# Kernel optimization log

Hardware: AMD Instinct MI355X
Metric: run time of the kernel (lower is better)

Reference implementation:

```python
import jax, jax.numpy as jnp
import numpy as np

N_NODES = 2048
N_PAIRS = 65536
D = 512
P = 16


def setup_inputs() -> dict:
    key = jax.random.key(0)
    ks = jax.random.split(key, 9)
    scale = 1.0 / np.sqrt(D)
    obj_feats = jax.random.normal(ks[0], (N_NODES, D), dtype=jnp.float32)
    union_feats = jax.random.normal(ks[1], (N_PAIRS, D), dtype=jnp.float32)
    pair_idxs = jax.random.randint(ks[2], (N_PAIRS, 2), 0, N_NODES, dtype=jnp.int64)
    ws_w = jax.random.uniform(ks[3], (D, D), jnp.float32, -scale, scale)
    ws_b = jax.random.uniform(ks[4], (D,), jnp.float32, -scale, scale)
    wo_w = jax.random.uniform(ks[5], (D, D), jnp.float32, -scale, scale)
    wo_b = jax.random.uniform(ks[6], (D,), jnp.float32, -scale, scale)
    w_w = jax.random.uniform(ks[7], (P, D), jnp.float32, -scale, scale)
    w_b = jax.random.uniform(ks[8], (P,), jnp.float32, -scale, scale)
    return {
        'obj_feats': obj_feats, 'union_feats': union_feats, 'pair_idxs': pair_idxs,
        'ws_w': ws_w, 'ws_b': ws_b, 'wo_w': wo_w, 'wo_b': wo_b, 'w_w': w_w, 'w_b': w_b,
    }


def reference(obj_feats, union_feats, pair_idxs, ws_w, ws_b, wo_w, wo_b, w_w, w_b):
    n = obj_feats.shape[0]
    p = w_w.shape[0]
    # node projections: [N, D]
    s = obj_feats @ ws_w.T + ws_b
    o = obj_feats @ wo_w.T + wo_b
    # gather pair features and fuse elementwise product: [E, D]
    prod = s[pair_idxs[:, 0]] * o[pair_idxs[:, 1]] * union_feats
    # project to p attention logits per pair: [E, p]
    atten_f = prod @ w_w.T + w_b
    # scatter into dense [N, N, p]
    atten = jnp.zeros((n, n, p), dtype=obj_feats.dtype)
    atten = atten.at[pair_idxs[:, 0], pair_idxs[:, 1]].add(atten_f)
    # mask diagonal with -1e4 and softmax over axis=1 (incoming nodes)
    atten = atten - jnp.eye(n, dtype=obj_feats.dtype)[:, :, None] * 10000.0
    return jax.nn.softmax(atten, axis=1)
```

## Files before the change

### kernel.cpp

```cpp
#include <hip/hip_runtime.h>
#include <hip/hip_bf16.h>

#define N_NODES 2048
#define N_PAIRS 65536
#define DIM 512
#define NP 16
#define SLOTS 96

typedef __attribute__((ext_vector_type(8))) short s16x8;
typedef __attribute__((ext_vector_type(8))) unsigned short u16x8;
typedef __attribute__((ext_vector_type(4))) float f32x4;

static __device__ __forceinline__ unsigned short f2bf(float x) {
    union { float f; unsigned int u; } v; v.f = x;
    unsigned int r = v.u + 0x7FFFu + ((v.u >> 16) & 1u);
    return (unsigned short)(r >> 16);
}
static __device__ __forceinline__ float bf2f(unsigned short u) {
    union { unsigned int u; float f; } v; v.u = ((unsigned int)u) << 16;
    return v.f;
}
static __device__ __forceinline__ u16x8 pack8(float4 a, float4 b) {
    u16x8 r;
    r[0]=f2bf(a.x); r[1]=f2bf(a.y); r[2]=f2bf(a.z); r[3]=f2bf(a.w);
    r[4]=f2bf(b.x); r[5]=f2bf(b.y); r[6]=f2bf(b.z); r[7]=f2bf(b.w);
    return r;
}

#define GBM 64
#define GBN 64
#define GBK 32
#define GSA 40

__global__ __launch_bounds__(256) void gemm_so(
    const float* __restrict__ A, const float* __restrict__ Ws, const float* __restrict__ bsv,
    const float* __restrict__ Wo, const float* __restrict__ bov,
    unsigned short* __restrict__ Sb, unsigned short* __restrict__ Ob)
{
    __shared__ unsigned short As[GBM*GSA];
    __shared__ unsigned short Bs[GBN*GSA];
    const int tid = threadIdx.x;
    const int m0 = blockIdx.y*GBM, n0 = blockIdx.x*GBN;
    const int ar = tid>>2, ac = (tid&3)*8;
    const float* Arow = A + (size_t)(m0+ar)*DIM + ac;
    const int nrow = n0 + ar;
    const float* Wrow = (nrow < DIM ? Ws + (size_t)nrow*DIM : Wo + (size_t)(nrow-DIM)*DIM) + ac;
    float4 a_r[2], b_r[2];
    a_r[0] = *(const float4*)(Arow);   a_r[1] = *(const float4*)(Arow+4);
    b_r[0] = *(const float4*)(Wrow);   b_r[1] = *(const float4*)(Wrow+4);

    const int lane = tid&63, wid = tid>>6;
    const int wm = (wid>>1)*32, wn = (wid&1)*32;
    const int fr = lane&15, ks8 = (lane>>4)*8;
    f32x4 acc[2][2] = {};
    for (int k0=0; k0<DIM; k0+=GBK) {
        *(u16x8*)&As[ar*GSA+ac] = pack8(a_r[0],a_r[1]);
        *(u16x8*)&Bs[ar*GSA+ac] = pack8(b_r[0],b_r[1]);
        __syncthreads();
        if (k0+GBK < DIM) {
            a_r[0] = *(const float4*)(Arow + k0+GBK);   a_r[1] = *(const float4*)(Arow + k0+GBK + 4);
            b_r[0] = *(const float4*)(Wrow + k0+GBK);   b_r[1] = *(const float4*)(Wrow + k0+GBK + 4);
        }
        s16x8 af[2], bfr[2];
        #pragma unroll
        for (int mi=0;mi<2;++mi) af[mi]  = *(const s16x8*)&As[(wm+mi*16+fr)*GSA + ks8];
        #pragma unroll
        for (int ni=0;ni<2;++ni) bfr[ni] = *(const s16x8*)&Bs[(wn+ni*16+fr)*GSA + ks8];
        #pragma unroll
        for (int mi=0;mi<2;++mi)
            #pragma unroll
            for (int ni=0;ni<2;++ni)
                acc[mi][ni] = __builtin_amdgcn_mfma_f32_16x16x32_bf16(af[mi], bfr[ni], acc[mi][ni], 0,0,0);
        __syncthreads();
    }
    const int rg = lane>>4;
    #pragma unroll
    for (int ni=0;ni<2;++ni) {
        const int n = n0 + wn + ni*16 + fr;
        const float bias = (n < DIM) ? bsv[n] : bov[n-DIM];
        unsigned short* dst = (n < DIM) ? (Sb + n) : (Ob + (n - DIM));
        #pragma unroll
        for (int mi=0;mi<2;++mi) {
            #pragma unroll
            for (int q=0;q<4;++q) {
                const int m = m0 + wm + mi*16 + rg*4 + q;
                dst[(size_t)m*DIM] = f2bf(acc[mi][ni][q] + bias);
            }
        }
    }
}

#define SP 520

__global__ __launch_bounds__(256) void pairproj_k(
    const unsigned short* __restrict__ Sb, const unsigned short* __restrict__ Ob,
    const float* __restrict__ U, const int* __restrict__ idx,
    const float* __restrict__ w_w, const float* __restrict__ w_b,
    int* __restrict__ rowcnt, int* __restrict__ rowj, float* __restrict__ rowv)
{
    __shared__ unsigned short P[4*16*SP];
    const int tid = threadIdx.x;
    const int lane = tid&63, wid = tid>>6;
    const int fr = lane&15, ks8 = (lane>>4)*8;
    s16x8 wreg[16];
    #pragma unroll
    for (int st=0;st<16;++st) {
        const float4* wp = (const float4*)(w_w + (size_t)fr*DIM + st*32 + ks8);
        u16x8 t = pack8(wp[0], wp[1]);
        wreg[st] = *(s16x8*)&t;
    }
    const float wbv = w_b[fr];
    unsigned short* Pw = &P[wid*16*SP];
    const int eb = blockIdx.x*128 + wid*32;
    for (int it=0; it<2; ++it) {
        const int e0 = eb + it*16;
        #pragma unroll 4
        for (int s8=0; s8<16; ++s8) {
            const int e = e0 + s8;
            const int i = idx[2*e], j = idx[2*e+1];
            u16x8 sv = *(const u16x8*)(Sb + (size_t)i*DIM + lane*8);
            u16x8 ov = *(const u16x8*)(Ob + (size_t)j*DIM + lane*8);
            const float4* up = (const float4*)(U + (size_t)e*DIM + lane*8);
            float4 u0 = up[0], u1 = up[1];
            float4 p0, p1;
            p0.x = bf2f(sv[0])*bf2f(ov[0])*u0.x;
            p0.y = bf2f(sv[1])*bf2f(ov[1])*u0.y;
            p0.z = bf2f(sv[2])*bf2f(ov[2])*u0.z;
            p0.w = bf2f(sv[3])*bf2f(ov[3])*u0.w;
            p1.x = bf2f(sv[4])*bf2f(ov[4])*u1.x;
            p1.y = bf2f(sv[5])*bf2f(ov[5])*u1.y;
            p1.z = bf2f(sv[6])*bf2f(ov[6])*u1.z;
            p1.w = bf2f(sv[7])*bf2f(ov[7])*u1.w;
            *(u16x8*)&Pw[s8*SP + lane*8] = pack8(p0, p1);
        }
        f32x4 acc = {0.f,0.f,0.f,0.f};
        #pragma unroll
        for (int st=0;st<16;++st) {
            s16x8 af = *(const s16x8*)&Pw[fr*SP + st*32 + ks8];
            acc = __builtin_amdgcn_mfma_f32_16x16x32_bf16(af, wreg[st], acc, 0,0,0);
        }
        int iv = 0, posv = 0;
        if (lane < 16) {
            const int e = e0 + lane;
            iv = idx[2*e];
            const int jv = idx[2*e + 1];
            posv = atomicAdd(&rowcnt[iv], 1);
            if (posv < SLOTS) rowj[iv*SLOTS + posv] = jv;
        }
        const int rg = lane>>4;
        #pragma unroll
        for (int q=0;q<4;++q) {
            const int pr = rg*4 + q;
            const int ip = __shfl(iv, pr, 64);
            const int pp = __shfl(posv, pr, 64);
            if (pp < SLOTS)
                rowv[((size_t)ip*SLOTS + pp)*NP + fr] = acc[q] + wbv;
        }
    }
}

__global__ __launch_bounds__(256) void softmax_k(
    const int* __restrict__ rowcnt, const int* __restrict__ rowj,
    const float* __restrict__ rowv, float* __restrict__ out)
{
    __shared__ __align__(16) float vals[SLOTS][NP];
    __shared__ int jcol[SLOTS];
    __shared__ unsigned char dead[SLOTS];
    __shared__ float red[16][17];
    __shared__ float mP[NP], invZ[NP], bg[NP];
    __shared__ int ndistinct;
    const int i = blockIdx.x;
    const int t = threadIdx.x;
    int c = rowcnt[i];
    if (c > SLOTS) c = SLOTS;

    if (t == 0) ndistinct = 0;
    for (int a = t; a < c; a += 256) {
        jcol[a] = rowj[i*SLOTS + a];
        dead[a] = 0;
        const float4* src = (const float4*)(rowv + ((size_t)i*SLOTS + a)*NP);
        float4* dst = (float4*)vals[a];
        dst[0] = src[0]; dst[1] = src[1]; dst[2] = src[2]; dst[3] = src[3];
    }
    __syncthreads();

    for (int a = t; a < c; a += 256) {
        int j = jcol[a];
        int first = a;
        for (int b = 0; b < a; ++b) if (jcol[b] == j) { first = b; break; }
        if (first != a) {
            dead[a] = 1;
            #pragma unroll
            for (int p = 0; p < NP; ++p) atomicAdd(&vals[first][p], vals[a][p]);
        }
    }
    __syncthreads();

    for (int a = t; a < c; a += 256)
        if (!dead[a] && jcol[a] != i) atomicAdd(&ndistinct, 1);
    __syncthreads();

    const int p = t & 15, ch = t >> 4;
    float pm = 0.f;
    for (int a = ch; a < c; a += 16)
        if (!dead[a] && jcol[a] != i) pm = fmaxf(pm, vals[a][p]);
    red[ch][p] = pm;
    __syncthreads();
    if (t < NP) {
        float m = 0.f;
        #pragma unroll
        for (int k = 0; k < 16; ++k) m = fmaxf(m, red[k][p]);
        mP[p] = m;
    }
    __syncthreads();
    {
        const float m = mP[p];
        float ps = 0.f;
        for (int a = ch; a < c; a += 16)
            if (!dead[a] && jcol[a] != i) ps += __expf(vals[a][p] - m);
        red[ch][p] = ps;
    }
    __syncthreads();
    if (t < NP) {
        float zs = 0.f;
        #pragma unroll
        for (int k = 0; k < 16; ++k) zs += red[k][p];
        const float m = mP[p];
        const float eb = __expf(-m);
        const float nbg = (float)(N_NODES - 1 - ndistinct);
        const float Z = zs + nbg * eb;
        const float iz = 1.0f / Z;
        invZ[p] = iz; bg[p] = eb * iz;
    }
    __syncthreads();

    const size_t rowbase = (size_t)i * N_NODES * NP;
    {
        const int g = t & 3;
        float4 b4 = make_float4(bg[g*4+0], bg[g*4+1], bg[g*4+2], bg[g*4+3]);
        float4* orow = (float4*)(out + rowbase);
        #pragma unroll 8
        for (int n = 0; n < 32; ++n) orow[t + 256 * n] = b4;
    }
    __syncthreads();

    for (int a = t; a < c; a += 256) {
        if (dead[a]) continue;
        const int j = jcol[a];
        float4* dst = (float4*)(out + rowbase + (size_t)j * NP);
        if (j == i) {
            float4 z = make_float4(0.f, 0.f, 0.f, 0.f);
            dst[0] = z; dst[1] = z; dst[2] = z; dst[3] = z;
        } else {
            #pragma unroll
            for (int q = 0; q < 4; ++q) {
                float4 v;
                v.x = __expf(vals[a][4*q+0] - mP[4*q+0]) * invZ[4*q+0];
                v.y = __expf(vals[a][4*q+1] - mP[4*q+1]) * invZ[4*q+1];
                v.z = __expf(vals[a][4*q+2] - mP[4*q+2]) * invZ[4*q+2];
                v.w = __expf(vals[a][4*q+3] - mP[4*q+3]) * invZ[4*q+3];
                dst[q] = v;
            }
        }
    }
    if (t == 0) {
        float4 z = make_float4(0.f, 0.f, 0.f, 0.f);
        float4* dst = (float4*)(out + rowbase + (size_t)i * NP);
        dst[0] = z; dst[1] = z; dst[2] = z; dst[3] = z;
    }
}

extern "C" void kernel_launch(void* const* d_in, const int* in_sizes, int n_in,
                              void* d_out, int out_size, void* d_ws, size_t ws_size,
                              hipStream_t stream)
{
    (void)in_sizes; (void)n_in; (void)out_size; (void)ws_size;
    const float* obj  = (const float*)d_in[0];
    const float* uni  = (const float*)d_in[1];
    const int*   idx  = (const int*)  d_in[2];
    const float* ws_w = (const float*)d_in[3];
    const float* ws_b = (const float*)d_in[4];
    const float* wo_w = (const float*)d_in[5];
    const float* wo_b = (const float*)d_in[6];
    const float* w_w  = (const float*)d_in[7];
    const float* w_b  = (const float*)d_in[8];
    float* out = (float*)d_out;

    unsigned short* Sb = (unsigned short*)d_ws;
    unsigned short* Ob = Sb + (size_t)N_NODES * DIM;
    float* rowv = (float*)(Ob + (size_t)N_NODES * DIM);
    int* rowj   = (int*)(rowv + (size_t)N_NODES * SLOTS * NP);
    int* rowcnt = rowj + (size_t)N_NODES * SLOTS;

    hipMemsetAsync(rowcnt, 0, N_NODES * sizeof(int), stream);
    gemm_so<<<dim3(1024/GBN, N_NODES/GBM), 256, 0, stream>>>(obj, ws_w, ws_b, wo_w, wo_b, Sb, Ob);
    pairproj_k<<<N_PAIRS/128, 256, 0, stream>>>(Sb, Ob, uni, idx, w_w, w_b, rowcnt, rowj, rowv);
    softmax_k<<<N_NODES, 256, 0, stream>>>(rowcnt, rowj, rowv, out);
}
```

Before: 130.9 us.

## Fuse pair projection and row softmax into persistent kernel with per-row readiness counters

```diff
diff --git a/kernel.cpp b/kernel.cpp
--- a/kernel.cpp
+++ b/kernel.cpp
@@ -6,6 +6,8 @@
 #define DIM 512
 #define NP 16
 #define SLOTS 96
+#define SP 520
+#define NCHUNKA (N_PAIRS/64)
 
 typedef __attribute__((ext_vector_type(8))) short s16x8;
 typedef __attribute__((ext_vector_type(8))) unsigned short u16x8;
@@ -90,183 +92,192 @@
     }
 }
 
-#define SP 520
-
-__global__ __launch_bounds__(256) void pairproj_k(
+__global__ __launch_bounds__(256) void hist_k(const int* __restrict__ idx, int* __restrict__ hist)
+{
+    int e = blockIdx.x * 256 + threadIdx.x;
+    atomicAdd(&hist[idx[2*e]], 1);
+}
+
+__global__ __launch_bounds__(128) void fused_k(
     const unsigned short* __restrict__ Sb, const unsigned short* __restrict__ Ob,
     const float* __restrict__ U, const int* __restrict__ idx,
     const float* __restrict__ w_w, const float* __restrict__ w_b,
-    int* __restrict__ rowcnt, int* __restrict__ rowj, float* __restrict__ rowv)
+    int* __restrict__ rowcnt, int* __restrict__ rowdone, const int* __restrict__ hist,
+    int* __restrict__ rowj, float* __restrict__ rowv,
+    int* __restrict__ tickets, float* __restrict__ out)
 {
-    __shared__ unsigned short P[4*16*SP];
+    __shared__ __align__(16) unsigned char smem[2*16*SP*2];
+    __shared__ int tkA, tkB, ndv;
+    __shared__ float mPv[NP], invZv[NP];
+
     const int tid = threadIdx.x;
-    const int lane = tid&63, wid = tid>>6;
-    const int fr = lane&15, ks8 = (lane>>4)*8;
-    s16x8 wreg[16];
-    #pragma unroll
-    for (int st=0;st<16;++st) {
-        const float4* wp = (const float4*)(w_w + (size_t)fr*DIM + st*32 + ks8);
-        u16x8 t = pack8(wp[0], wp[1]);
-        wreg[st] = *(s16x8*)&t;
+    const int lane = tid & 63, wid = tid >> 6;
+    const int fr = lane & 15, ks8 = (lane >> 4) * 8;
+
+    {
+        s16x8 wreg[16];
+        #pragma unroll
+        for (int st=0;st<16;++st) {
+            const float4* wp = (const float4*)(w_w + (size_t)fr*DIM + st*32 + ks8);
+            u16x8 t = pack8(wp[0], wp[1]);
+            wreg[st] = *(s16x8*)&t;
+        }
+        const float wbv = w_b[fr];
+        unsigned short* P = (unsigned short*)smem;
+        unsigned short* Pw = &P[wid*16*SP];
+        for (;;) {
+            __syncthreads();
+            if (tid == 0) tkA = atomicAdd(&tickets[0], 1);
+            __syncthreads();
+            const int chunk = tkA;
+            if (chunk >= NCHUNKA) break;
+            const int eb = chunk*64 + wid*32;
+            for (int it = 0; it < 2; ++it) {
+                const int e0 = eb + it*16;
+                #pragma unroll 4
+                for (int s8=0; s8<16; ++s8) {
+                    const int e = e0 + s8;
+                    const int i = idx[2*e], j = idx[2*e+1];
+                    u16x8 sv = *(const u16x8*)(Sb + (size_t)i*DIM + lane*8);
+                    u16x8 ov = *(const u16x8*)(Ob + (size_t)j*DIM + lane*8);
+                    const float4* up = (const float4*)(U + (size_t)e*DIM + lane*8);
+                    float4 u0 = up[0], u1 = up[1];
+                    float4 p0, p1;
+                    p0.x = bf2f(sv[0])*bf2f(ov[0])*u0.x;
+                    p0.y = bf2f(sv[1])*bf2f(ov[1])*u0.y;
+                    p0.z = bf2f(sv[2])*bf2f(ov[2])*u0.z;
+                    p0.w = bf2f(sv[3])*bf2f(ov[3])*u0.w;
+                    p1.x = bf2f(sv[4])*bf2f(ov[4])*u1.x;
+                    p1.y = bf2f(sv[5])*bf2f(ov[5])*u1.y;
+                    p1.z = bf2f(sv[6])*bf2f(ov[6])*u1.z;
+                    p1.w = bf2f(sv[7])*bf2f(ov[7])*u1.w;
+                    *(u16x8*)&Pw[s8*SP + lane*8] = pack8(p0, p1);
+                }
+                f32x4 acc = {0.f,0.f,0.f,0.f};
+                #pragma unroll
+                for (int st=0;st<16;++st) {
+                    s16x8 af = *(const s16x8*)&Pw[fr*SP + st*32 + ks8];
+                    acc = __builtin_amdgcn_mfma_f32_16x16x32_bf16(af, wreg[st], acc, 0,0,0);
+                }
+                int iv = 0, posv = 0;
+                if (lane < 16) {
+                    const int e = e0 + lane;
+                    iv = idx[2*e];
+                    const int jv = idx[2*e + 1];
+                    posv = atomicAdd(&rowcnt[iv], 1);
+                    if (posv < SLOTS) rowj[iv*SLOTS + posv] = jv;
+                }
+                const int rg = lane>>4;
+                #pragma unroll
+                for (int q=0;q<4;++q) {
+                    const int pr = rg*4 + q;
+                    const int ip = __shfl(iv, pr, 64);
+                    const int pp = __shfl(posv, pr, 64);
+                    if (pp < SLOTS)
+                        rowv[((size_t)ip*SLOTS + pp)*NP + fr] = acc[q] + wbv;
+                }
+                __threadfence();
+                if (lane < 16)
+                    __hip_atomic_fetch_add(&rowdone[iv], 1, __ATOMIC_RELEASE, __HIP_MEMORY_SCOPE_AGENT);
+            }
+        }
     }
-    const float wbv = w_b[fr];
-    unsigned short* Pw = &P[wid*16*SP];
-    const int eb = blockIdx.x*128 + wid*32;
-    for (int it=0; it<2; ++it) {
-        const int e0 = eb + it*16;
-        #pragma unroll 4
-        for (int s8=0; s8<16; ++s8) {
-            const int e = e0 + s8;
-            const int i = idx[2*e], j = idx[2*e+1];
-            u16x8 sv = *(const u16x8*)(Sb + (size_t)i*DIM + lane*8);
-            u16x8 ov = *(const u16x8*)(Ob + (size_t)j*DIM + lane*8);
-            const float4* up = (const float4*)(U + (size_t)e*DIM + lane*8);
-            float4 u0 = up[0], u1 = up[1];
-            float4 p0, p1;
-            p0.x = bf2f(sv[0])*bf2f(ov[0])*u0.x;
-            p0.y = bf2f(sv[1])*bf2f(ov[1])*u0.y;
-            p0.z = bf2f(sv[2])*bf2f(ov[2])*u0.z;
-            p0.w = bf2f(sv[3])*bf2f(ov[3])*u0.w;
-            p1.x = bf2f(sv[4])*bf2f(ov[4])*u1.x;
-            p1.y = bf2f(sv[5])*bf2f(ov[5])*u1.y;
-            p1.z = bf2f(sv[6])*bf2f(ov[6])*u1.z;
-            p1.w = bf2f(sv[7])*bf2f(ov[7])*u1.w;
-            *(u16x8*)&Pw[s8*SP + lane*8] = pack8(p0, p1);
-        }
-        f32x4 acc = {0.f,0.f,0.f,0.f};
-        #pragma unroll
-        for (int st=0;st<16;++st) {
-            s16x8 af = *(const s16x8*)&Pw[fr*SP + st*32 + ks8];
-            acc = __builtin_amdgcn_mfma_f32_16x16x32_bf16(af, wreg[st], acc, 0,0,0);
-        }
-        int iv = 0, posv = 0;
-        if (lane < 16) {
-            const int e = e0 + lane;
-            iv = idx[2*e];
-            const int jv = idx[2*e + 1];
-            posv = atomicAdd(&rowcnt[iv], 1);
-            if (posv < SLOTS) rowj[iv*SLOTS + posv] = jv;
-        }
-        const int rg = lane>>4;
-        #pragma unroll
-        for (int q=0;q<4;++q) {
-            const int pr = rg*4 + q;
-            const int ip = __shfl(iv, pr, 64);
-            const int pp = __shfl(posv, pr, 64);
-            if (pp < SLOTS)
-                rowv[((size_t)ip*SLOTS + pp)*NP + fr] = acc[q] + wbv;
-        }
-    }
-}
-
-__global__ __launch_bounds__(256) void softmax_k(
-    const int* __restrict__ rowcnt, const int* __restrict__ rowj,
-    const float* __restrict__ rowv, float* __restrict__ out)
-{
-    __shared__ __align__(16) float vals[SLOTS][NP];
-    __shared__ int jcol[SLOTS];
-    __shared__ unsigned char dead[SLOTS];
-    __shared__ float red[16][17];
-    __shared__ float mP[NP], invZ[NP], bg[NP];
-    __shared__ int ndistinct;
-    const int i = blockIdx.x;
-    const int t = threadIdx.x;
-    int c = rowcnt[i];
-    if (c > SLOTS) c = SLOTS;
-
-    if (t == 0) ndistinct = 0;
-    for (int a = t; a < c; a += 256) {
-        jcol[a] = rowj[i*SLOTS + a];
-        dead[a] = 0;
-        const float4* src = (const float4*)(rowv + ((size_t)i*SLOTS + a)*NP);
-        float4* dst = (float4*)vals[a];
-        dst[0] = src[0]; dst[1] = src[1]; dst[2] = src[2]; dst[3] = src[3];
-    }
-    __syncthreads();
-
-    for (int a = t; a < c; a += 256) {
-        int j = jcol[a];
-        int first = a;
-        for (int b = 0; b < a; ++b) if (jcol[b] == j) { first = b; break; }
-        if (first != a) {
-            dead[a] = 1;
+
+    float* vals = (float*)smem;
+    int*   jcol = (int*)(smem + 98*NP*4);
+    unsigned char* deadf = (unsigned char*)(smem + 98*NP*4 + SLOTS*4);
+    unsigned char* cmap  = deadf + SLOTS;
+    float* red = (float*)(smem + 8800);
+
+    for (;;) {
+        __syncthreads();
+        if (tid == 0) tkB = atomicAdd(&tickets[1], 1);
+        __syncthreads();
+        const int r = tkB;
+        if (r >= N_NODES) break;
+        const int expect = hist[r];
+        {
+            int g = 0;
+            while (__hip_atomic_load(&rowdone[r], __ATOMIC_ACQUIRE, __HIP_MEMORY_SCOPE_AGENT) < expect
+                   && g < (1<<25)) { ++g; __builtin_amdgcn_s_sleep(2); }
+        }
+        int c = expect; if (c > SLOTS) c = SLOTS;
+        if (tid == 0) ndv = 0;
+        for (int n = tid; n < N_NODES; n += 128) cmap[n] = (unsigned char)SLOTS;
+        for (int a = tid; a < c; a += 128) {
+            jcol[a] = rowj[r*SLOTS + a];
+            deadf[a] = 0;
+            const float4* src = (const float4*)(rowv + ((size_t)r*SLOTS + a)*NP);
+            float4* dst = (float4*)&vals[a*NP];
+            dst[0]=src[0]; dst[1]=src[1]; dst[2]=src[2]; dst[3]=src[3];
+        }
+        __syncthreads();
+        for (int a = tid; a < c; a += 128) {
+            int j = jcol[a]; int first = a;
+            for (int b = 0; b < a; ++b) if (jcol[b] == j) { first = b; break; }
+            if (first != a) {
+                deadf[a] = 1;
+                #pragma unroll
+                for (int p = 0; p < NP; ++p) atomicAdd(&vals[first*NP+p], vals[a*NP+p]);
+            }
+        }
+        __syncthreads();
+        for (int a = tid; a < c; a += 128)
+            if (!deadf[a] && jcol[a] != r) atomicAdd(&ndv, 1);
+        __syncthreads();
+        const int p = tid & 15, ch = tid >> 4;
+        float pm = 0.f;
+        for (int a = ch; a < c; a += 8)
+            if (!deadf[a] && jcol[a] != r) pm = fmaxf(pm, vals[a*NP+p]);
+        red[ch*17+p] = pm;
+        __syncthreads();
+        if (tid < NP) {
+            float m = 0.f;
             #pragma unroll
-            for (int p = 0; p < NP; ++p) atomicAdd(&vals[first][p], vals[a][p]);
-        }
-    }
-    __syncthreads();
-
-    for (int a = t; a < c; a += 256)
-        if (!dead[a] && jcol[a] != i) atomicAdd(&ndistinct, 1);
-    __syncthreads();
-
-    const int p = t & 15, ch = t >> 4;
-    float pm = 0.f;
-    for (int a = ch; a < c; a += 16)
-        if (!dead[a] && jcol[a] != i) pm = fmaxf(pm, vals[a][p]);
-    red[ch][p] = pm;
-    __syncthreads();
-    if (t < NP) {
-        float m = 0.f;
-        #pragma unroll
-        for (int k = 0; k < 16; ++k) m = fmaxf(m, red[k][p]);
-        mP[p] = m;
-    }
-    __syncthreads();
-    {
-        const float m = mP[p];
-        float ps = 0.f;
-        for (int a = ch; a < c; a += 16)
-            if (!dead[a] && jcol[a] != i) ps += __expf(vals[a][p] - m);
-        red[ch][p] = ps;
-    }
-    __syncthreads();
-    if (t < NP) {
-        float zs = 0.f;
-        #pragma unroll
-        for (int k = 0; k < 16; ++k) zs += red[k][p];
-        const float m = mP[p];
-        const float eb = __expf(-m);
-        const float nbg = (float)(N_NODES - 1 - ndistinct);
-        const float Z = zs + nbg * eb;
-        const float iz = 1.0f / Z;
-        invZ[p] = iz; bg[p] = eb * iz;
-    }
-    __syncthreads();
-
-    const size_t rowbase = (size_t)i * N_NODES * NP;
-    {
-        const int g = t & 3;
-        float4 b4 = make_float4(bg[g*4+0], bg[g*4+1], bg[g*4+2], bg[g*4+3]);
-        float4* orow = (float4*)(out + rowbase);
+            for (int k = 0; k < 8; ++k) m = fmaxf(m, red[k*17+tid]);
+            mPv[tid] = m;
+        }
+        __syncthreads();
+        {
+            const float m = mPv[p];
+            float ps = 0.f;
+            for (int a = ch; a < c; a += 8)
+                if (!deadf[a] && jcol[a] != r) ps += __expf(vals[a*NP+p] - m);
+            red[ch*17+p] = ps;
+        }
+        __syncthreads();
+        if (tid < NP) {
+            float zs = 0.f;
+            #pragma unroll
+            for (int k = 0; k < 8; ++k) zs += red[k*17+tid];
+            const float m = mPv[tid];
+            const float eb2 = __expf(-m);
+            const float Z = zs + (float)(N_NODES - 1 - ndv) * eb2;
+            const float iz = 1.0f / Z;
+            invZv[tid] = iz;
+            vals[SLOTS*NP + tid] = eb2 * iz;
+            vals[(SLOTS+1)*NP + tid] = 0.f;
+        }
+        __syncthreads();
+        for (int a = tid; a < c; a += 128) {
+            if (!deadf[a] && jcol[a] != r) {
+                #pragma unroll
+                for (int p2 = 0; p2 < NP; ++p2)
+                    vals[a*NP+p2] = __expf(vals[a*NP+p2] - mPv[p2]) * invZv[p2];
+                cmap[jcol[a]] = (unsigned char)a;
+            }
+        }
+        __syncthreads();
+        if (tid == 0) cmap[r] = (unsigned char)(SLOTS+1);
+        __syncthreads();
+        float4* orow = (float4*)(out + (size_t)r * N_NODES * NP);
+        const float4* v4 = (const float4*)vals;
         #pragma unroll 8
-        for (int n = 0; n < 32; ++n) orow[t + 256 * n] = b4;
-    }
-    __syncthreads();
-
-    for (int a = t; a < c; a += 256) {
-        if (dead[a]) continue;
-        const int j = jcol[a];
-        float4* dst = (float4*)(out + rowbase + (size_t)j * NP);
-        if (j == i) {
-            float4 z = make_float4(0.f, 0.f, 0.f, 0.f);
-            dst[0] = z; dst[1] = z; dst[2] = z; dst[3] = z;
-        } else {
-            #pragma unroll
-            for (int q = 0; q < 4; ++q) {
-                float4 v;
-                v.x = __expf(vals[a][4*q+0] - mP[4*q+0]) * invZ[4*q+0];
-                v.y = __expf(vals[a][4*q+1] - mP[4*q+1]) * invZ[4*q+1];
-                v.z = __expf(vals[a][4*q+2] - mP[4*q+2]) * invZ[4*q+2];
-                v.w = __expf(vals[a][4*q+3] - mP[4*q+3]) * invZ[4*q+3];
-                dst[q] = v;
-            }
-        }
-    }
-    if (t == 0) {
-        float4 z = make_float4(0.f, 0.f, 0.f, 0.f);
-        float4* dst = (float4*)(out + rowbase + (size_t)i * NP);
-        dst[0] = z; dst[1] = z; dst[2] = z; dst[3] = z;
+        for (int n = 0; n < 64; ++n) {
+            const int i4 = tid + 128*n;
+            const int col = i4 >> 2, q = i4 & 3;
+            orow[i4] = v4[(int)cmap[col]*4 + q];
+        }
     }
 }
 
@@ -288,12 +299,16 @@
 
     unsigned short* Sb = (unsigned short*)d_ws;
     unsigned short* Ob = Sb + (size_t)N_NODES * DIM;
-    float* rowv = (float*)(Ob + (size_t)N_NODES * DIM);
-    int* rowj   = (int*)(rowv + (size_t)N_NODES * SLOTS * NP);
-    int* rowcnt = rowj + (size_t)N_NODES * SLOTS;
-
-    hipMemsetAsync(rowcnt, 0, N_NODES * sizeof(int), stream);
+    float* rowv  = (float*)(Ob + (size_t)N_NODES * DIM);
+    int* rowj    = (int*)(rowv + (size_t)N_NODES * SLOTS * NP);
+    int* rowcnt  = rowj + (size_t)N_NODES * SLOTS;
+    int* rowdone = rowcnt + N_NODES;
+    int* hist    = rowdone + N_NODES;
+    int* tickets = hist + N_NODES;
+
+    hipMemsetAsync(rowcnt, 0, (3 * N_NODES + 8) * sizeof(int), stream);
+    hist_k<<<N_PAIRS/256, 256, 0, stream>>>(idx, hist);
     gemm_so<<<dim3(1024/GBN, N_NODES/GBM), 256, 0, stream>>>(obj, ws_w, ws_b, wo_w, wo_b, Sb, Ob);
-    pairproj_k<<<N_PAIRS/128, 256, 0, stream>>>(Sb, Ob, uni, idx, w_w, w_b, rowcnt, rowj, rowv);
-    softmax_k<<<N_NODES, 256, 0, stream>>>(rowcnt, rowj, rowv, out);
-}
+    fused_k<<<1024, 128, 0, stream>>>(Sb, Ob, uni, idx, w_w, w_b,
+                                      rowcnt, rowdone, hist, rowj, rowv, tickets, out);
+}
```

Result: slower. 432.9 us (+230.7%).

## Feed MFMA directly from gathered pair rows and write softmax rows via column map

Applied to the files above, without the earlier changes.

```diff
diff --git a/kernel.cpp b/kernel.cpp
--- a/kernel.cpp
+++ b/kernel.cpp
@@ -90,72 +90,63 @@
     }
 }
 
-#define SP 520
-
 __global__ __launch_bounds__(256) void pairproj_k(
     const unsigned short* __restrict__ Sb, const unsigned short* __restrict__ Ob,
     const float* __restrict__ U, const int* __restrict__ idx,
     const float* __restrict__ w_w, const float* __restrict__ w_b,
     int* __restrict__ rowcnt, int* __restrict__ rowj, float* __restrict__ rowv)
 {
-    __shared__ unsigned short P[4*16*SP];
     const int tid = threadIdx.x;
-    const int lane = tid&63, wid = tid>>6;
-    const int fr = lane&15, ks8 = (lane>>4)*8;
+    const int lane = tid & 63, wid = tid >> 6;
+    const int fr = lane & 15, ks8 = (lane >> 4) * 8;
     s16x8 wreg[16];
     #pragma unroll
-    for (int st=0;st<16;++st) {
+    for (int st = 0; st < 16; ++st) {
         const float4* wp = (const float4*)(w_w + (size_t)fr*DIM + st*32 + ks8);
         u16x8 t = pack8(wp[0], wp[1]);
         wreg[st] = *(s16x8*)&t;
     }
     const float wbv = w_b[fr];
-    unsigned short* Pw = &P[wid*16*SP];
-    const int eb = blockIdx.x*128 + wid*32;
-    for (int it=0; it<2; ++it) {
-        const int e0 = eb + it*16;
-        #pragma unroll 4
-        for (int s8=0; s8<16; ++s8) {
-            const int e = e0 + s8;
-            const int i = idx[2*e], j = idx[2*e+1];
-            u16x8 sv = *(const u16x8*)(Sb + (size_t)i*DIM + lane*8);
-            u16x8 ov = *(const u16x8*)(Ob + (size_t)j*DIM + lane*8);
-            const float4* up = (const float4*)(U + (size_t)e*DIM + lane*8);
-            float4 u0 = up[0], u1 = up[1];
-            float4 p0, p1;
-            p0.x = bf2f(sv[0])*bf2f(ov[0])*u0.x;
-            p0.y = bf2f(sv[1])*bf2f(ov[1])*u0.y;
-            p0.z = bf2f(sv[2])*bf2f(ov[2])*u0.z;
-            p0.w = bf2f(sv[3])*bf2f(ov[3])*u0.w;
-            p1.x = bf2f(sv[4])*bf2f(ov[4])*u1.x;
-            p1.y = bf2f(sv[5])*bf2f(ov[5])*u1.y;
-            p1.z = bf2f(sv[6])*bf2f(ov[6])*u1.z;
-            p1.w = bf2f(sv[7])*bf2f(ov[7])*u1.w;
-            *(u16x8*)&Pw[s8*SP + lane*8] = pack8(p0, p1);
-        }
-        f32x4 acc = {0.f,0.f,0.f,0.f};
-        #pragma unroll
-        for (int st=0;st<16;++st) {
-            s16x8 af = *(const s16x8*)&Pw[fr*SP + st*32 + ks8];
-            acc = __builtin_amdgcn_mfma_f32_16x16x32_bf16(af, wreg[st], acc, 0,0,0);
-        }
-        int iv = 0, posv = 0;
-        if (lane < 16) {
-            const int e = e0 + lane;
-            iv = idx[2*e];
-            const int jv = idx[2*e + 1];
-            posv = atomicAdd(&rowcnt[iv], 1);
-            if (posv < SLOTS) rowj[iv*SLOTS + posv] = jv;
-        }
-        const int rg = lane>>4;
-        #pragma unroll
-        for (int q=0;q<4;++q) {
-            const int pr = rg*4 + q;
-            const int ip = __shfl(iv, pr, 64);
-            const int pp = __shfl(posv, pr, 64);
-            if (pp < SLOTS)
-                rowv[((size_t)ip*SLOTS + pp)*NP + fr] = acc[q] + wbv;
-        }
+
+    const int e = blockIdx.x * 64 + wid * 16 + fr;
+    const int i = idx[2*e], j = idx[2*e + 1];
+    const unsigned short* sp = Sb + (size_t)i * DIM;
+    const unsigned short* op = Ob + (size_t)j * DIM;
+    const float*          up = U  + (size_t)e * DIM;
+
+    f32x4 acc = {0.f, 0.f, 0.f, 0.f};
+    #pragma unroll 4
+    for (int st = 0; st < 16; ++st) {
+        const int k = st*32 + ks8;
+        u16x8 sv = *(const u16x8*)(sp + k);
+        u16x8 ov = *(const u16x8*)(op + k);
+        float4 u0 = *(const float4*)(up + k);
+        float4 u1 = *(const float4*)(up + k + 4);
+        float4 p0, p1;
+        p0.x = bf2f(sv[0])*bf2f(ov[0])*u0.x;
+        p0.y = bf2f(sv[1])*bf2f(ov[1])*u0.y;
+        p0.z = bf2f(sv[2])*bf2f(ov[2])*u0.z;
+        p0.w = bf2f(sv[3])*bf2f(ov[3])*u0.w;
+        p1.x = bf2f(sv[4])*bf2f(ov[4])*u1.x;
+        p1.y = bf2f(sv[5])*bf2f(ov[5])*u1.y;
+        p1.z = bf2f(sv[6])*bf2f(ov[6])*u1.z;
+        p1.w = bf2f(sv[7])*bf2f(ov[7])*u1.w;
+        u16x8 pa = pack8(p0, p1);
+        acc = __builtin_amdgcn_mfma_f32_16x16x32_bf16(*(s16x8*)&pa, wreg[st], acc, 0,0,0);
+    }
+    int posv = 0;
+    if (lane < 16) {
+        posv = atomicAdd(&rowcnt[i], 1);
+        if (posv < SLOTS) rowj[i*SLOTS + posv] = j;
+    }
+    const int rg = lane >> 4;
+    #pragma unroll
+    for (int q = 0; q < 4; ++q) {
+        const int pr = rg*4 + q;
+        const int ip = __shfl(i, pr, 64);
+        const int pp = __shfl(posv, pr, 64);
+        if (pp < SLOTS)
+            rowv[((size_t)ip*SLOTS + pp)*NP + fr] = acc[q] + wbv;
     }
 }
 
@@ -163,110 +154,97 @@
     const int* __restrict__ rowcnt, const int* __restrict__ rowj,
     const float* __restrict__ rowv, float* __restrict__ out)
 {
-    __shared__ __align__(16) float vals[SLOTS][NP];
+    __shared__ __align__(16) float vals[(SLOTS+2)*NP];
     __shared__ int jcol[SLOTS];
-    __shared__ unsigned char dead[SLOTS];
+    __shared__ unsigned char deadf[SLOTS];
+    __shared__ unsigned char cmap[N_NODES];
     __shared__ float red[16][17];
-    __shared__ float mP[NP], invZ[NP], bg[NP];
-    __shared__ int ndistinct;
-    const int i = blockIdx.x;
+    __shared__ float mPv[NP], invZv[NP];
+    __shared__ int ndv;
+    const int r = blockIdx.x;
     const int t = threadIdx.x;
-    int c = rowcnt[i];
+    int c = rowcnt[r];
     if (c > SLOTS) c = SLOTS;
 
-    if (t == 0) ndistinct = 0;
+    if (t == 0) ndv = 0;
+    for (int n = t; n < N_NODES; n += 256) cmap[n] = (unsigned char)SLOTS;
     for (int a = t; a < c; a += 256) {
-        jcol[a] = rowj[i*SLOTS + a];
-        dead[a] = 0;
-        const float4* src = (const float4*)(rowv + ((size_t)i*SLOTS + a)*NP);
-        float4* dst = (float4*)vals[a];
-        dst[0] = src[0]; dst[1] = src[1]; dst[2] = src[2]; dst[3] = src[3];
+        jcol[a] = rowj[r*SLOTS + a];
+        deadf[a] = 0;
+        const float4* src = (const float4*)(rowv + ((size_t)r*SLOTS + a)*NP);
+        float4* dst = (float4*)&vals[a*NP];
+        dst[0]=src[0]; dst[1]=src[1]; dst[2]=src[2]; dst[3]=src[3];
     }
     __syncthreads();
 
     for (int a = t; a < c; a += 256) {
-        int j = jcol[a];
-        int first = a;
+        int j = jcol[a]; int first = a;
         for (int b = 0; b < a; ++b) if (jcol[b] == j) { first = b; break; }
         if (first != a) {
-            dead[a] = 1;
-            #pragma unroll
-            for (int p = 0; p < NP; ++p) atomicAdd(&vals[first][p], vals[a][p]);
-        }
-    }
-    __syncthreads();
-
+            deadf[a] = 1;
+            #pragma unroll
+            for (int p = 0; p < NP; ++p) atomicAdd(&vals[first*NP+p], vals[a*NP+p]);
+        }
+    }
+    __syncthreads();
     for (int a = t; a < c; a += 256)
-        if (!dead[a] && jcol[a] != i) atomicAdd(&ndistinct, 1);
+        if (!deadf[a] && jcol[a] != r) atomicAdd(&ndv, 1);
     __syncthreads();
 
     const int p = t & 15, ch = t >> 4;
     float pm = 0.f;
     for (int a = ch; a < c; a += 16)
-        if (!dead[a] && jcol[a] != i) pm = fmaxf(pm, vals[a][p]);
+        if (!deadf[a] && jcol[a] != r) pm = fmaxf(pm, vals[a*NP+p]);
     red[ch][p] = pm;
     __syncthreads();
     if (t < NP) {
         float m = 0.f;
         #pragma unroll
-        for (int k = 0; k < 16; ++k) m = fmaxf(m, red[k][p]);
-        mP[p] = m;
+        for (int k = 0; k < 16; ++k) m = fmaxf(m, red[k][t]);
+        mPv[t] = m;
     }
     __syncthreads();
     {
-        const float m = mP[p];
+        const float m = mPv[p];
         float ps = 0.f;
         for (int a = ch; a < c; a += 16)
-            if (!dead[a] && jcol[a] != i) ps += __expf(vals[a][p] - m);
+            if (!deadf[a] && jcol[a] != r) ps += __expf(vals[a*NP+p] - m);
         red[ch][p] = ps;
     }
     __syncthreads();
     if (t < NP) {
         float zs = 0.f;
         #pragma unroll
-        for (int k = 0; k < 16; ++k) zs += red[k][p];
-        const float m = mP[p];
+        for (int k = 0; k < 16; ++k) zs += red[k][t];
+        const float m = mPv[t];
         const float eb = __expf(-m);
-        const float nbg = (float)(N_NODES - 1 - ndistinct);
-        const float Z = zs + nbg * eb;
+        const float Z = zs + (float)(N_NODES - 1 - ndv) * eb;
         const float iz = 1.0f / Z;
-        invZ[p] = iz; bg[p] = eb * iz;
-    }
-    __syncthreads();
-
-    const size_t rowbase = (size_t)i * N_NODES * NP;
-    {
-        const int g = t & 3;
-        float4 b4 = make_float4(bg[g*4+0], bg[g*4+1], bg[g*4+2], bg[g*4+3]);
-        float4* orow = (float4*)(out + rowbase);
-        #pragma unroll 8
-        for (int n = 0; n < 32; ++n) orow[t + 256 * n] = b4;
+        invZv[t] = iz;
+        vals[SLOTS*NP + t] = eb * iz;
+        vals[(SLOTS+1)*NP + t] = 0.f;
     }
     __syncthreads();
 
     for (int a = t; a < c; a += 256) {
-        if (dead[a]) continue;
-        const int j = jcol[a];
-        float4* dst = (float4*)(out + rowbase + (size_t)j * NP);
-        if (j == i) {
-            float4 z = make_float4(0.f, 0.f, 0.f, 0.f);
-            dst[0] = z; dst[1] = z; dst[2] = z; dst[3] = z;
-        } else {
-            #pragma unroll
-            for (int q = 0; q < 4; ++q) {
-                float4 v;
-                v.x = __expf(vals[a][4*q+0] - mP[4*q+0]) * invZ[4*q+0];
-                v.y = __expf(vals[a][4*q+1] - mP[4*q+1]) * invZ[4*q+1];
-                v.z = __expf(vals[a][4*q+2] - mP[4*q+2]) * invZ[4*q+2];
-                v.w = __expf(vals[a][4*q+3] - mP[4*q+3]) * invZ[4*q+3];
-                dst[q] = v;
-            }
-        }
-    }
-    if (t == 0) {
-        float4 z = make_float4(0.f, 0.f, 0.f, 0.f);
-        float4* dst = (float4*)(out + rowbase + (size_t)i * NP);
-        dst[0] = z; dst[1] = z; dst[2] = z; dst[3] = z;
+        if (!deadf[a] && jcol[a] != r) {
+            #pragma unroll
+            for (int p2 = 0; p2 < NP; ++p2)
+                vals[a*NP+p2] = __expf(vals[a*NP+p2] - mPv[p2]) * invZv[p2];
+            cmap[jcol[a]] = (unsigned char)a;
+        }
+    }
+    __syncthreads();
+    if (t == 0) cmap[r] = (unsigned char)(SLOTS+1);
+    __syncthreads();
+
+    float4* orow = (float4*)(out + (size_t)r * N_NODES * NP);
+    const float4* v4 = (const float4*)vals;
+    #pragma unroll 8
+    for (int n = 0; n < 32; ++n) {
+        const int i4 = t + 256*n;
+        const int col = i4 >> 2, q = i4 & 3;
+        orow[i4] = v4[(int)cmap[col]*4 + q];
     }
 }
 
@@ -288,12 +266,12 @@
 
     unsigned short* Sb = (unsigned short*)d_ws;
     unsigned short* Ob = Sb + (size_t)N_NODES * DIM;
-    float* rowv = (float*)(Ob + (size_t)N_NODES * DIM);
-    int* rowj   = (int*)(rowv + (size_t)N_NODES * SLOTS * NP);
-    int* rowcnt = rowj + (size_t)N_NODES * SLOTS;
+    float* rowv  = (float*)(Ob + (size_t)N_NODES * DIM);
+    int* rowj    = (int*)(rowv + (size_t)N_NODES * SLOTS * NP);
+    int* rowcnt  = rowj + (size_t)N_NODES * SLOTS;
 
     hipMemsetAsync(rowcnt, 0, N_NODES * sizeof(int), stream);
     gemm_so<<<dim3(1024/GBN, N_NODES/GBM), 256, 0, stream>>>(obj, ws_w, ws_b, wo_w, wo_b, Sb, Ob);
-    pairproj_k<<<N_PAIRS/128, 256, 0, stream>>>(Sb, Ob, uni, idx, w_w, w_b, rowcnt, rowj, rowv);
+    pairproj_k<<<N_PAIRS/64, 256, 0, stream>>>(Sb, Ob, uni, idx, w_w, w_b, rowcnt, rowj, rowv);
     softmax_k<<<N_NODES, 256, 0, stream>>>(rowcnt, rowj, rowv, out);
 }
```

Measured after the change: 149.2 us. +14.0%, slower.
